# Performance work log

Measured on AMD Instinct MI355X. Metric: run time of the kernel, lower is better.

The kernel has to match this reference:

```python
import jax, jax.numpy as jnp
import numpy as np

B, T, D = 4096, 200, 64
H1, H2 = 128, 64


def setup_inputs() -> dict:
    key = jax.random.key(0)
    ks = jax.random.split(key, 9)
    def glorot(k, shape):
        fan_in, fan_out = shape[0], shape[1]
        lim = float(np.sqrt(6.0 / (fan_in + fan_out)))
        return jax.random.uniform(k, shape, jnp.float32, -lim, lim)
    return {
        "candidate_embedding": jax.random.normal(ks[0], (B, D), jnp.float32),
        "history_embeddings": jax.random.normal(ks[1], (B, T, D), jnp.float32),
        "mask": jax.random.randint(ks[2], (B, T), 0, 2, jnp.int32),
        "W1": glorot(ks[3], (4 * D, H1)),
        "b1": jnp.zeros((H1,), jnp.float32),
        "W2": glorot(ks[4], (H1, H2)),
        "b2": jnp.zeros((H2,), jnp.float32),
        "W3": glorot(ks[5], (H2, 1)),
        "b3": jnp.zeros((1,), jnp.float32),
    }


def reference(candidate_embedding, history_embeddings, mask, W1, b1, W2, b2, W3, b3):
    # candidate: [B, D] -> broadcast to [B, T, D]
    cand = candidate_embedding[:, None, :]  # [B, 1, D]
    cand = jnp.broadcast_to(cand, history_embeddings.shape)
    # DIN feature concat: [B, T, 4D]
    feats = jnp.concatenate(
        [cand, history_embeddings, cand - history_embeddings, cand * history_embeddings],
        axis=-1,
    )
    # small MLP scorer per position
    h = jax.nn.relu(jnp.einsum("btf,fh->bth", feats, W1) + b1)
    h = jax.nn.relu(jnp.einsum("btf,fh->bth", h, W2) + b2)
    scores = (jnp.einsum("btf,fo->bto", h, W3) + b3)[..., 0]  # [B, T]
    # masked softmax over T
    scores = jnp.where(mask == 0, jnp.float32(-1e9), scores)
    weights = jax.nn.softmax(scores, axis=1)  # [B, T]
    # weighted sum over history: [B, D]
    return jnp.einsum("btd,bt->bd", history_embeddings, weights)
```

## Files before the change

kernel.cpp:

```cpp
#include <hip/hip_runtime.h>
#include <hip/hip_bf16.h>

#define NB 4096
#define NT 200
#define ND 64
#define NH1 128
#define NH2 64

#define WS_WX 0
#define WS_WC 16384
#define WS_W2 24576
#define WS_B1 32768
#define WS_B2 32896
#define WS_W3 32960
#define WS_B3 33024

__device__ __align__(16) float  g_wxt[8192];
__device__ __align__(16) float  g_wdt[8192];
__device__ __align__(16) __bf16 g_w2ts[8192];
__device__ __align__(16) __bf16 g_w2tsh[8192];
__device__ __align__(16) __bf16 g_w2tsl[8192];

typedef __bf16 bf16x8 __attribute__((ext_vector_type(8)));
typedef __bf16 bf16x4 __attribute__((ext_vector_type(4)));
typedef float  f32x4  __attribute__((ext_vector_type(4)));

__device__ __forceinline__ float ldany(const void* p, int i, int bf) {
    if (bf) return __bfloat162float(((const __hip_bfloat16*)p)[i]);
    return ((const float*)p)[i];
}

__global__ __launch_bounds__(256) void prep_kernel(
    const void* W1, const void* b1, const void* W2, const void* b2,
    const void* W3, const void* b3, int* flag_out, float* F) {
    __shared__ int votes;
    int tid = threadIdx.x;
    if (tid == 0) votes = 0;
    __syncthreads();
    {
        const unsigned* w1u = (const unsigned*)W1;
        unsigned w = w1u[tid];
        unsigned lo = w & 0xFFFFu;
        unsigned e = (lo >> 7) & 0xFFu;
        if (lo == 0u || (e >= 96u && e <= 124u)) atomicAdd(&votes, 1);
    }
    __syncthreads();
    int bf = (votes >= 160) ? 1 : 0;
    if (blockIdx.x == 0 && tid == 0) flag_out[0] = bf;

    int gtid = blockIdx.x * blockDim.x + tid;
    int gstride = gridDim.x * blockDim.x;

    for (int e = gtid; e < 8192; e += gstride) {
        int k = e >> 7, j = e & 127;
        float w1b = ldany(W1, (64 + k) * 128 + j, bf);
        float w1c = ldany(W1, (128 + k) * 128 + j, bf);
        float w1a = ldany(W1, k * 128 + j, bf);
        float w1d = ldany(W1, (192 + k) * 128 + j, bf);
        float wx = w1b - w1c;
        F[WS_WX + e] = wx;
        F[WS_WX + 8192 + e] = w1d;
        F[WS_WC + e] = w1a + w1c;
        g_wxt[j * 64 + k] = wx;
        g_wdt[j * 64 + k] = w1d;
        float w2v = ldany(W2, e, bf);
        F[WS_W2 + e] = w2v;
        int j2 = e & 63, k2 = e >> 6;
        int so = j2 * 128 + (k2 ^ ((j2 & 15) << 3));
        g_w2ts[so] = (__bf16)w2v;
        __bf16 w2h = (__bf16)w2v;
        g_w2tsh[so] = w2h;
        g_w2tsl[so] = (__bf16)(w2v - (float)w2h);
    }
    for (int e = gtid; e < 128; e += gstride) F[WS_B1 + e] = ldany(b1, e, bf);
    for (int e = gtid; e < 64; e += gstride) {
        F[WS_B2 + e] = ldany(b2, e, bf);
        F[WS_W3 + e] = ldany(W3, e, bf);
    }
    if (gtid == 0) F[WS_B3] = ldany(b3, 0, bf);
}

__device__ __forceinline__ void compute_chunk_bf(
    int w, int lane, int tbase, int b, const int* mask,
    const __bf16* sH, const __bf16* sWhi, const __bf16* sWlo,
    __bf16* h1hi, __bf16* h1lo,
    const float* cbias, const float* b2s, const float* W3s, float b3v,
    float* ss)
{
    const int lq = lane >> 4, lr = lane & 15;
    const int t0 = 16 * w;
    const int ar = t0 + lr;
    const int asw = (ar & 7) << 3;
    const bf16x8 a0 = *(const bf16x8*)&sH[ar * 64 + ((lq * 8) ^ asw)];
    const bf16x8 a1 = *(const bf16x8*)&sH[ar * 64 + ((32 + lq * 8) ^ asw)];
    __syncthreads();

    f32x4 acc2[4];
#pragma unroll
    for (int n = 0; n < 4; n++) {
        const float bb = b2s[n * 16 + lr];
        acc2[n] = (f32x4){bb, bb, bb, bb};
    }

#pragma unroll
    for (int half = 0; half < 2; half++) {
#pragma unroll
        for (int n = 0; n < 4; n++) {
            const int col = half * 64 + n * 16 + lr;
            const int bsw = (col & 7) << 3;
            const int wb = col * 64;
            const float cb = cbias[col];
            f32x4 c = {cb, cb, cb, cb};
            const bf16x8 bh0 = *(const bf16x8*)&sWhi[wb + ((lq * 8) ^ bsw)];
            const bf16x8 bh1 = *(const bf16x8*)&sWhi[wb + ((32 + lq * 8) ^ bsw)];
            const bf16x8 bl0 = *(const bf16x8*)&sWlo[wb + ((lq * 8) ^ bsw)];
            const bf16x8 bl1 = *(const bf16x8*)&sWlo[wb + ((32 + lq * 8) ^ bsw)];
            c = __builtin_amdgcn_mfma_f32_16x16x32_bf16(a0, bh0, c, 0, 0, 0);
            c = __builtin_amdgcn_mfma_f32_16x16x32_bf16(a1, bh1, c, 0, 0, 0);
            c = __builtin_amdgcn_mfma_f32_16x16x32_bf16(a0, bl0, c, 0, 0, 0);
            c = __builtin_amdgcn_mfma_f32_16x16x32_bf16(a1, bl1, c, 0, 0, 0);
#pragma unroll
            for (int r = 0; r < 4; r++) {
                const int row = t0 + lq * 4 + r;
                const int lcol = n * 16 + lr;
                const int hoff = row * 64 + (lcol ^ ((row & 7) << 3));
                float v = fmaxf(c[r], 0.f);
                __bf16 hi = (__bf16)v;
                h1hi[hoff] = hi;
                h1lo[hoff] = (__bf16)(v - (float)hi);
            }
        }
        __syncthreads();
#pragma unroll
        for (int s = 0; s < 2; s++) {
            const int kl = s * 32 + lq * 8;
            const int kg = half * 64 + kl;
            const int hoff2 = (t0 + lr) * 64 + (kl ^ ((lr & 7) << 3));
            const bf16x8 ah = *(const bf16x8*)&h1hi[hoff2];
            const bf16x8 al = *(const bf16x8*)&h1lo[hoff2];
#pragma unroll
            for (int n = 0; n < 4; n++) {
                const int col = n * 16 + lr;
                const int gso = col * 128 + (kg ^ ((col & 15) << 3));
                const bf16x8 bb = *(const bf16x8*)&g_w2ts[gso];
                acc2[n] = __builtin_amdgcn_mfma_f32_16x16x32_bf16(ah, bb, acc2[n], 0, 0, 0);
                acc2[n] = __builtin_amdgcn_mfma_f32_16x16x32_bf16(al, bb, acc2[n], 0, 0, 0);
            }
        }
        if (half == 0) __syncthreads();
    }

#pragma unroll
    for (int r = 0; r < 4; r++) {
        float p = 0.f;
#pragma unroll
        for (int n = 0; n < 4; n++)
            p = fmaf(fmaxf(acc2[n][r], 0.f), W3s[n * 16 + lr], p);
        p += __shfl_xor(p, 1);
        p += __shfl_xor(p, 2);
        p += __shfl_xor(p, 4);
        p += __shfl_xor(p, 8);
        const int gt = tbase + t0 + lq * 4 + r;
        if (lr == 0 && gt < NT)
            ss[gt] = (mask[(long)b * NT + gt] != 0) ? (p + b3v) : -1e9f;
    }
}

__global__ __launch_bounds__(512, 4) void attn_bf16_kernel(
    const void* cand, const void* hist, const int* mask,
    const int* flag_p, const float* F, void* out)
{
    if (flag_p[0] == 0) return;

    __shared__ __align__(16) __bf16 sWhi[8192];
    __shared__ __align__(16) __bf16 sWlo[8192];
    __shared__ __align__(16) __bf16 uBuf[16384];
    __shared__ float cbias[128];
    __shared__ float cs[64], W3s[64], b2s[64];
    __shared__ float ss[NT];
    __shared__ float sred[8];
    __shared__ float b3s;

    const int tid = threadIdx.x;
    const int b = blockIdx.x;
    const int w = tid >> 6, lane = tid & 63;
    const __hip_bfloat16* hp = (const __hip_bfloat16*)hist;

    __bf16* sH = uBuf;
    __bf16* h1hi = uBuf;
    __bf16* h1lo = uBuf + 8192;

    if (tid < 64) {
        cs[tid] = __bfloat162float(((const __hip_bfloat16*)cand)[(long)b * 64 + tid]);
        W3s[tid] = F[WS_W3 + tid];
        b2s[tid] = F[WS_B2 + tid];
    }
    if (tid == 0) b3s = F[WS_B3];
#pragma unroll
    for (int i = 0; i < 2; i++) {
        const int idx = tid + i * 512;
        const int t = idx >> 3, q = idx & 7;
        uint4 v = *(const uint4*)(hp + ((long)b * NT + t) * 64 + q * 8);
        *(uint4*)&sH[t * 64 + ((q * 8) ^ ((t & 7) << 3))] = v;
    }
    __syncthreads();

#pragma unroll
    for (int i = 0; i < 4; i++) {
        const int e4 = tid + i * 512;
        const int j = e4 >> 4, k4 = (e4 & 15) << 2;
        const float4 wx = *(const float4*)&g_wxt[e4 * 4];
        const float4 wd = *(const float4*)&g_wdt[e4 * 4];
        bf16x4 hi4, lo4;
        float v0 = fmaf(cs[k4 + 0], wd.x, wx.x);
        float v1 = fmaf(cs[k4 + 1], wd.y, wx.y);
        float v2 = fmaf(cs[k4 + 2], wd.z, wx.z);
        float v3 = fmaf(cs[k4 + 3], wd.w, wx.w);
        hi4[0] = (__bf16)v0; lo4[0] = (__bf16)(v0 - (float)hi4[0]);
        hi4[1] = (__bf16)v1; lo4[1] = (__bf16)(v1 - (float)hi4[1]);
        hi4[2] = (__bf16)v2; lo4[2] = (__bf16)(v2 - (float)hi4[2]);
        hi4[3] = (__bf16)v3; lo4[3] = (__bf16)(v3 - (float)hi4[3]);
        const int off = j * 64 + (k4 ^ ((j & 7) << 3));
        *(bf16x4*)&sWhi[off] = hi4;
        *(bf16x4*)&sWlo[off] = lo4;
    }
    {
        const int j = tid >> 2, kq = (tid & 3) << 4;
        float a = 0.f;
#pragma unroll
        for (int k2 = 0; k2 < 16; k2++)
            a = fmaf(cs[kq + k2], F[WS_WC + (kq + k2) * 128 + j], a);
        a += __shfl_xor(a, 1);
        a += __shfl_xor(a, 2);
        if ((tid & 3) == 0) cbias[j] = a + F[WS_B1 + j];
    }
    uint4 c1a, c1b = {0, 0, 0, 0};
    {
        const int t = 128 + (tid >> 3), q = tid & 7;
        c1a = *(const uint4*)(hp + ((long)b * NT + t) * 64 + q * 8);
    }
    if (tid < 64) {
        const int t = 192 + (tid >> 3), q = tid & 7;
        c1b = *(const uint4*)(hp + ((long)b * NT + t) * 64 + q * 8);
    }
    __builtin_amdgcn_sched_barrier(0);
    __syncthreads();

    const float b3v = b3s;
    compute_chunk_bf(w, lane, 0, b, mask, sH, sWhi, sWlo, h1hi, h1lo,
                     cbias, b2s, W3s, b3v, ss);
    __syncthreads();

    {
        const int t = tid >> 3, q = tid & 7;
        *(uint4*)&sH[t * 64 + ((q * 8) ^ ((t & 7) << 3))] = c1a;
    }
    if (tid < 64) {
        const int t = 64 + (tid >> 3), q = tid & 7;
        *(uint4*)&sH[t * 64 + ((q * 8) ^ ((t & 7) << 3))] = c1b;
    }
    if (tid < 64) {
        const int t = 72 + (tid >> 3), q = tid & 7;
        uint4 z = {0, 0, 0, 0};
        *(uint4*)&sH[t * 64 + ((q * 8) ^ ((t & 7) << 3))] = z;
    }
    __syncthreads();

    compute_chunk_bf(w, lane, 128, b, mask, sH, sWhi, sWlo, h1hi, h1lo,
                     cbias, b2s, W3s, b3v, ss);
    __syncthreads();

    float v = (tid < NT) ? ss[tid] : -3.0e38f;
    if (tid < 256) {
        float m = v;
#pragma unroll
        for (int o = 32; o; o >>= 1) m = fmaxf(m, __shfl_xor(m, o));
        if ((tid & 63) == 0) sred[tid >> 6] = m;
    }
    __syncthreads();
    const float M = fmaxf(fmaxf(sred[0], sred[1]), fmaxf(sred[2], sred[3]));
    float p = (tid < NT) ? __expf(v - M) : 0.f;
    if (tid < 256) {
        float s2 = p;
#pragma unroll
        for (int o = 32; o; o >>= 1) s2 += __shfl_xor(s2, o);
        if ((tid & 63) == 0) sred[4 + (tid >> 6)] = s2;
    }
    __syncthreads();
    const float S = sred[4] + sred[5] + sred[6] + sred[7];
    if (tid < NT) ss[tid] = p / S;
    __syncthreads();

    float* part = (float*)uBuf;
    const int d = tid & 63, g = tid >> 6;
    float acc = 0.f;
    for (int t = g; t < NT; t += 8)
        acc = fmaf(ss[t], __bfloat162float(hp[((long)b * NT + t) * 64 + d]), acc);
    part[g * 65 + d] = acc;
    __syncthreads();
    if (tid < 64) {
        float o = 0.f;
#pragma unroll
        for (int g2 = 0; g2 < 8; g2++) o += part[g2 * 65 + tid];
        ((__hip_bfloat16*)out)[b * 64 + tid] = __float2bfloat16(o);
    }
}

__device__ __forceinline__ void compute_chunk_f32(
    int w, int lane, int tbase, int b, const int* mask,
    const __bf16* sHhi, const __bf16* sHlo,
    const __bf16* sWhi, const __bf16* sWlo,
    __bf16* h1hi, __bf16* h1lo,
    const float* cbias, const float* b2s, const float* W3s, float b3v,
    float* ss)
{
    const int lq = lane >> 4, lr = lane & 15;
    const int t0 = 16 * w;
    const int ar = t0 + lr;
    const int asw = (ar & 7) << 3;
    const bf16x8 a0h = *(const bf16x8*)&sHhi[ar * 64 + ((lq * 8) ^ asw)];
    const bf16x8 a1h = *(const bf16x8*)&sHhi[ar * 64 + ((32 + lq * 8) ^ asw)];
    const bf16x8 a0l = *(const bf16x8*)&sHlo[ar * 64 + ((lq * 8) ^ asw)];
    const bf16x8 a1l = *(const bf16x8*)&sHlo[ar * 64 + ((32 + lq * 8) ^ asw)];
    __syncthreads();

    f32x4 acc2[4];
#pragma unroll
    for (int n = 0; n < 4; n++) {
        const float bb = b2s[n * 16 + lr];
        acc2[n] = (f32x4){bb, bb, bb, bb};
    }

#pragma unroll
    for (int half = 0; half < 2; half++) {
#pragma unroll
        for (int n = 0; n < 4; n++) {
            const int col = half * 64 + n * 16 + lr;
            const int bsw = (col & 7) << 3;
            const int wb = col * 64;
            const float cb = cbias[col];
            f32x4 c = {cb, cb, cb, cb};
            const bf16x8 bh0 = *(const bf16x8*)&sWhi[wb + ((lq * 8) ^ bsw)];
            const bf16x8 bh1 = *(const bf16x8*)&sWhi[wb + ((32 + lq * 8) ^ bsw)];
            const bf16x8 bl0 = *(const bf16x8*)&sWlo[wb + ((lq * 8) ^ bsw)];
            const bf16x8 bl1 = *(const bf16x8*)&sWlo[wb + ((32 + lq * 8) ^ bsw)];
            c = __builtin_amdgcn_mfma_f32_16x16x32_bf16(a0h, bh0, c, 0, 0, 0);
            c = __builtin_amdgcn_mfma_f32_16x16x32_bf16(a1h, bh1, c, 0, 0, 0);
            c = __builtin_amdgcn_mfma_f32_16x16x32_bf16(a0l, bh0, c, 0, 0, 0);
            c = __builtin_amdgcn_mfma_f32_16x16x32_bf16(a1l, bh1, c, 0, 0, 0);
            c = __builtin_amdgcn_mfma_f32_16x16x32_bf16(a0h, bl0, c, 0, 0, 0);
            c = __builtin_amdgcn_mfma_f32_16x16x32_bf16(a1h, bl1, c, 0, 0, 0);
#pragma unroll
            for (int r = 0; r < 4; r++) {
                const int row = t0 + lq * 4 + r;
                const int lcol = n * 16 + lr;
                const int hoff = row * 64 + (lcol ^ ((row & 7) << 3));
                float v = fmaxf(c[r], 0.f);
                __bf16 hi = (__bf16)v;
                h1hi[hoff] = hi;
                h1lo[hoff] = (__bf16)(v - (float)hi);
            }
        }
        __syncthreads();
#pragma unroll
        for (int s = 0; s < 2; s++) {
            const int kl = s * 32 + lq * 8;
            const int kg = half * 64 + kl;
            const int hoff2 = (t0 + lr) * 64 + (kl ^ ((lr & 7) << 3));
            const bf16x8 ah = *(const bf16x8*)&h1hi[hoff2];
            const bf16x8 al = *(const bf16x8*)&h1lo[hoff2];
#pragma unroll
            for (int n = 0; n < 4; n++) {
                const int col = n * 16 + lr;
                const int gso = col * 128 + (kg ^ ((col & 15) << 3));
                const bf16x8 bh = *(const bf16x8*)&g_w2tsh[gso];
                const bf16x8 bl = *(const bf16x8*)&g_w2tsl[gso];
                acc2[n] = __builtin_amdgcn_mfma_f32_16x16x32_bf16(ah, bh, acc2[n], 0, 0, 0);
                acc2[n] = __builtin_amdgcn_mfma_f32_16x16x32_bf16(al, bh, acc2[n], 0, 0, 0);
                acc2[n] = __builtin_amdgcn_mfma_f32_16x16x32_bf16(ah, bl, acc2[n], 0, 0, 0);
            }
        }
        if (half == 0) __syncthreads();
    }

#pragma unroll
    for (int r = 0; r < 4; r++) {
        float p = 0.f;
#pragma unroll
        for (int n = 0; n < 4; n++)
            p = fmaf(fmaxf(acc2[n][r], 0.f), W3s[n * 16 + lr], p);
        p += __shfl_xor(p, 1);
        p += __shfl_xor(p, 2);
        p += __shfl_xor(p, 4);
        p += __shfl_xor(p, 8);
        const int gt = tbase + t0 + lq * 4 + r;
        if (lr == 0 && gt < NT)
            ss[gt] = (mask[(long)b * NT + gt] != 0) ? (p + b3v) : -1e9f;
    }
}

__global__ __launch_bounds__(512, 4) void attn_f32_kernel(
    const void* cand, const void* hist, const int* mask,
    const int* flag_p, const float* F, void* out)
{
    if (flag_p[0] != 0) return;

    __shared__ __align__(16) __bf16 sWhi[8192];
    __shared__ __align__(16) __bf16 sWlo[8192];
    __shared__ __align__(16) __bf16 uBuf[16384];
    __shared__ float cbias[128];
    __shared__ float cs[64], W3s[64], b2s[64];
    __shared__ float ss[NT];
    __shared__ float sred[8];
    __shared__ float b3s;

    const int tid = threadIdx.x;
    const int b = blockIdx.x;
    const int w = tid >> 6, lane = tid & 63;
    const float* hf = (const float*)hist;

    __bf16* sHhi = uBuf;
    __bf16* sHlo = uBuf + 8192;
    __bf16* h1hi = uBuf;
    __bf16* h1lo = uBuf + 8192;

    if (tid < 64) {
        cs[tid] = ((const float*)cand)[(long)b * 64 + tid];
        W3s[tid] = F[WS_W3 + tid];
        b2s[tid] = F[WS_B2 + tid];
    }
    if (tid == 0) b3s = F[WS_B3];
#pragma unroll
    for (int i = 0; i < 4; i++) {
        const int e4 = tid + i * 512;
        const int t = e4 >> 4, k = (e4 & 15) * 4;
        float4 v = *(const float4*)&hf[((long)b * NT + t) * 64 + k];
        bf16x4 hi4, lo4;
        hi4[0] = (__bf16)v.x; lo4[0] = (__bf16)(v.x - (float)hi4[0]);
        hi4[1] = (__bf16)v.y; lo4[1] = (__bf16)(v.y - (float)hi4[1]);
        hi4[2] = (__bf16)v.z; lo4[2] = (__bf16)(v.z - (float)hi4[2]);
        hi4[3] = (__bf16)v.w; lo4[3] = (__bf16)(v.w - (float)hi4[3]);
        const int pos = ((k & 56) ^ ((t & 7) << 3)) | (k & 4);
        *(bf16x4*)&sHhi[t * 64 + pos] = hi4;
        *(bf16x4*)&sHlo[t * 64 + pos] = lo4;
    }
    __syncthreads();

#pragma unroll
    for (int i = 0; i < 4; i++) {
        const int e4 = tid + i * 512;
        const int j = e4 >> 4, k4 = (e4 & 15) << 2;
        const float4 wx = *(const float4*)&g_wxt[e4 * 4];
        const float4 wd = *(const float4*)&g_wdt[e4 * 4];
        bf16x4 hi4, lo4;
        float v0 = fmaf(cs[k4 + 0], wd.x, wx.x);
        float v1 = fmaf(cs[k4 + 1], wd.y, wx.y);
        float v2 = fmaf(cs[k4 + 2], wd.z, wx.z);
        float v3 = fmaf(cs[k4 + 3], wd.w, wx.w);
        hi4[0] = (__bf16)v0; lo4[0] = (__bf16)(v0 - (float)hi4[0]);
        hi4[1] = (__bf16)v1; lo4[1] = (__bf16)(v1 - (float)hi4[1]);
        hi4[2] = (__bf16)v2; lo4[2] = (__bf16)(v2 - (float)hi4[2]);
        hi4[3] = (__bf16)v3; lo4[3] = (__bf16)(v3 - (float)hi4[3]);
        const int off = j * 64 + (k4 ^ ((j & 7) << 3));
        *(bf16x4*)&sWhi[off] = hi4;
        *(bf16x4*)&sWlo[off] = lo4;
    }
    {
        const int j = tid >> 2, kq = (tid & 3) << 4;
        float a = 0.f;
#pragma unroll
        for (int k2 = 0; k2 < 16; k2++)
            a = fmaf(cs[kq + k2], F[WS_WC + (kq + k2) * 128 + j], a);
        a += __shfl_xor(a, 1);
        a += __shfl_xor(a, 2);
        if ((tid & 3) == 0) cbias[j] = a + F[WS_B1 + j];
    }
    float4 c1a0, c1a1, c1b = {0.f, 0.f, 0.f, 0.f};
    {
        int e4 = tid;
        int tl = e4 >> 4, k = (e4 & 15) * 4;
        c1a0 = *(const float4*)&hf[((long)b * NT + 128 + tl) * 64 + k];
        e4 = tid + 512;
        tl = e4 >> 4; k = (e4 & 15) * 4;
        c1a1 = *(const float4*)&hf[((long)b * NT + 128 + tl) * 64 + k];
    }
    if (tid < 128) {
        const int e4 = 1024 + tid;
        const int tl = e4 >> 4, k = (e4 & 15) * 4;
        c1b = *(const float4*)&hf[((long)b * NT + 128 + tl) * 64 + k];
    }
    __builtin_amdgcn_sched_barrier(0);
    __syncthreads();

    const float b3v = b3s;
    compute_chunk_f32(w, lane, 0, b, mask, sHhi, sHlo, sWhi, sWlo,
                      h1hi, h1lo, cbias, b2s, W3s, b3v, ss);
    __syncthreads();

    {
        int e4 = tid;
        int tl = e4 >> 4, k = (e4 & 15) * 4;
        int pos = ((k & 56) ^ ((tl & 7) << 3)) | (k & 4);
        bf16x4 hi4, lo4;
        hi4[0] = (__bf16)c1a0.x; lo4[0] = (__bf16)(c1a0.x - (float)hi4[0]);
        hi4[1] = (__bf16)c1a0.y; lo4[1] = (__bf16)(c1a0.y - (float)hi4[1]);
        hi4[2] = (__bf16)c1a0.z; lo4[2] = (__bf16)(c1a0.z - (float)hi4[2]);
        hi4[3] = (__bf16)c1a0.w; lo4[3] = (__bf16)(c1a0.w - (float)hi4[3]);
        *(bf16x4*)&sHhi[tl * 64 + pos] = hi4;
        *(bf16x4*)&sHlo[tl * 64 + pos] = lo4;
        e4 = tid + 512;
        tl = e4 >> 4; k = (e4 & 15) * 4;
        pos = ((k & 56) ^ ((tl & 7) << 3)) | (k & 4);
        hi4[0] = (__bf16)c1a1.x; lo4[0] = (__bf16)(c1a1.x - (float)hi4[0]);
        hi4[1] = (__bf16)c1a1.y; lo4[1] = (__bf16)(c1a1.y - (float)hi4[1]);
        hi4[2] = (__bf16)c1a1.z; lo4[2] = (__bf16)(c1a1.z - (float)hi4[2]);
        hi4[3] = (__bf16)c1a1.w; lo4[3] = (__bf16)(c1a1.w - (float)hi4[3]);
        *(bf16x4*)&sHhi[tl * 64 + pos] = hi4;
        *(bf16x4*)&sHlo[tl * 64 + pos] = lo4;
    }
    if (tid < 128) {
        const int e4 = 1024 + tid;
        const int tl = e4 >> 4, k = (e4 & 15) * 4;
        const int pos = ((k & 56) ^ ((tl & 7) << 3)) | (k & 4);
        bf16x4 hi4, lo4;
        hi4[0] = (__bf16)c1b.x; lo4[0] = (__bf16)(c1b.x - (float)hi4[0]);
        hi4[1] = (__bf16)c1b.y; lo4[1] = (__bf16)(c1b.y - (float)hi4[1]);
        hi4[2] = (__bf16)c1b.z; lo4[2] = (__bf16)(c1b.z - (float)hi4[2]);
        hi4[3] = (__bf16)c1b.w; lo4[3] = (__bf16)(c1b.w - (float)hi4[3]);
        *(bf16x4*)&sHhi[tl * 64 + pos] = hi4;
        *(bf16x4*)&sHlo[tl * 64 + pos] = lo4;
    }
    if (tid < 128) {
        const int tl = 72 + (tid >> 4), k = (tid & 15) * 4;
        const int pos = ((k & 56) ^ ((tl & 7) << 3)) | (k & 4);
        bf16x4 z;
        z[0] = (__bf16)0.f; z[1] = (__bf16)0.f; z[2] = (__bf16)0.f; z[3] = (__bf16)0.f;
        *(bf16x4*)&sHhi[tl * 64 + pos] = z;
        *(bf16x4*)&sHlo[tl * 64 + pos] = z;
    }
    __syncthreads();

    compute_chunk_f32(w, lane, 128, b, mask, sHhi, sHlo, sWhi, sWlo,
                      h1hi, h1lo, cbias, b2s, W3s, b3v, ss);
    __syncthreads();

    float v = (tid < NT) ? ss[tid] : -3.0e38f;
    if (tid < 256) {
        float m = v;
#pragma unroll
        for (int o = 32; o; o >>= 1) m = fmaxf(m, __shfl_xor(m, o));
        if ((tid & 63) == 0) sred[tid >> 6] = m;
    }
    __syncthreads();
    const float M = fmaxf(fmaxf(sred[0], sred[1]), fmaxf(sred[2], sred[3]));
    float p = (tid < NT) ? __expf(v - M) : 0.f;
    if (tid < 256) {
        float s2 = p;
#pragma unroll
        for (int o = 32; o; o >>= 1) s2 += __shfl_xor(s2, o);
        if ((tid & 63) == 0) sred[4 + (tid >> 6)] = s2;
    }
    __syncthreads();
    const float S = sred[4] + sred[5] + sred[6] + sred[7];
    if (tid < NT) ss[tid] = p / S;
    __syncthreads();

    float* part = (float*)uBuf;
    const int d = tid & 63, g = tid >> 6;
    float acc = 0.f;
    for (int t = g; t < NT; t += 8)
        acc = fmaf(ss[t], hf[((long)b * NT + t) * 64 + d], acc);
    part[g * 65 + d] = acc;
    __syncthreads();
    if (tid < 64) {
        float o = 0.f;
#pragma unroll
        for (int g2 = 0; g2 < 8; g2++) o += part[g2 * 65 + tid];
        ((float*)out)[b * 64 + tid] = o;
    }
}

extern "C" void kernel_launch(void* const* d_in, const int* in_sizes, int n_in,
                              void* d_out, int out_size, void* d_ws, size_t ws_size,
                              hipStream_t stream) {
    const void* cand = d_in[0];
    const void* hist = d_in[1];
    const int* mask = (const int*)d_in[2];
    const void* W1 = d_in[3];
    const void* b1 = d_in[4];
    const void* W2 = d_in[5];
    const void* b2 = d_in[6];
    const void* W3 = d_in[7];
    const void* b3 = d_in[8];

    int* flag = (int*)d_ws;
    float* F = (float*)((char*)d_ws + 256);

    prep_kernel<<<32, 256, 0, stream>>>(W1, b1, W2, b2, W3, b3, flag, F);
    attn_f32_kernel<<<NB, 512, 0, stream>>>(cand, hist, mask, flag, F, d_out);
    attn_bf16_kernel<<<NB, 512, 0, stream>>>(cand, hist, mask, flag, F, d_out);
}
```

Baseline: 611.0 us.

## Shrink blocks to 256 threads and process history in 64-row chunks with prefetch

Both attention kernels drop from 512 to 256 threads per block and walk the 200 history rows in four 64-row chunks instead of two 128-row chunks. The next chunk is prefetched from global memory into registers while the current chunk's MLP runs. Shared memory for the activation buffer is halved and launch bounds change to (256,3), aiming at more resident blocks per CU and better latency hiding. The cost is more barriers per block and serial chunk iterations within each block.

New measurement: 776.1 us. 1.27x slower.

```diff
diff --git a/kernel.cpp b/kernel.cpp
--- a/kernel.cpp
+++ b/kernel.cpp
@@ -80,93 +80,7 @@
     if (gtid == 0) F[WS_B3] = ldany(b3, 0, bf);
 }
 
-__device__ __forceinline__ void compute_chunk_bf(
-    int w, int lane, int tbase, int b, const int* mask,
-    const __bf16* sH, const __bf16* sWhi, const __bf16* sWlo,
-    __bf16* h1hi, __bf16* h1lo,
-    const float* cbias, const float* b2s, const float* W3s, float b3v,
-    float* ss)
-{
-    const int lq = lane >> 4, lr = lane & 15;
-    const int t0 = 16 * w;
-    const int ar = t0 + lr;
-    const int asw = (ar & 7) << 3;
-    const bf16x8 a0 = *(const bf16x8*)&sH[ar * 64 + ((lq * 8) ^ asw)];
-    const bf16x8 a1 = *(const bf16x8*)&sH[ar * 64 + ((32 + lq * 8) ^ asw)];
-    __syncthreads();
-
-    f32x4 acc2[4];
-#pragma unroll
-    for (int n = 0; n < 4; n++) {
-        const float bb = b2s[n * 16 + lr];
-        acc2[n] = (f32x4){bb, bb, bb, bb};
-    }
-
-#pragma unroll
-    for (int half = 0; half < 2; half++) {
-#pragma unroll
-        for (int n = 0; n < 4; n++) {
-            const int col = half * 64 + n * 16 + lr;
-            const int bsw = (col & 7) << 3;
-            const int wb = col * 64;
-            const float cb = cbias[col];
-            f32x4 c = {cb, cb, cb, cb};
-            const bf16x8 bh0 = *(const bf16x8*)&sWhi[wb + ((lq * 8) ^ bsw)];
-            const bf16x8 bh1 = *(const bf16x8*)&sWhi[wb + ((32 + lq * 8) ^ bsw)];
-            const bf16x8 bl0 = *(const bf16x8*)&sWlo[wb + ((lq * 8) ^ bsw)];
-            const bf16x8 bl1 = *(const bf16x8*)&sWlo[wb + ((32 + lq * 8) ^ bsw)];
-            c = __builtin_amdgcn_mfma_f32_16x16x32_bf16(a0, bh0, c, 0, 0, 0);
-            c = __builtin_amdgcn_mfma_f32_16x16x32_bf16(a1, bh1, c, 0, 0, 0);
-            c = __builtin_amdgcn_mfma_f32_16x16x32_bf16(a0, bl0, c, 0, 0, 0);
-            c = __builtin_amdgcn_mfma_f32_16x16x32_bf16(a1, bl1, c, 0, 0, 0);
-#pragma unroll
-            for (int r = 0; r < 4; r++) {
-                const int row = t0 + lq * 4 + r;
-                const int lcol = n * 16 + lr;
-                const int hoff = row * 64 + (lcol ^ ((row & 7) << 3));
-                float v = fmaxf(c[r], 0.f);
-                __bf16 hi = (__bf16)v;
-                h1hi[hoff] = hi;
-                h1lo[hoff] = (__bf16)(v - (float)hi);
-            }
-        }
-        __syncthreads();
-#pragma unroll
-        for (int s = 0; s < 2; s++) {
-            const int kl = s * 32 + lq * 8;
-            const int kg = half * 64 + kl;
-            const int hoff2 = (t0 + lr) * 64 + (kl ^ ((lr & 7) << 3));
-            const bf16x8 ah = *(const bf16x8*)&h1hi[hoff2];
-            const bf16x8 al = *(const bf16x8*)&h1lo[hoff2];
-#pragma unroll
-            for (int n = 0; n < 4; n++) {
-                const int col = n * 16 + lr;
-                const int gso = col * 128 + (kg ^ ((col & 15) << 3));
-                const bf16x8 bb = *(const bf16x8*)&g_w2ts[gso];
-                acc2[n] = __builtin_amdgcn_mfma_f32_16x16x32_bf16(ah, bb, acc2[n], 0, 0, 0);
-                acc2[n] = __builtin_amdgcn_mfma_f32_16x16x32_bf16(al, bb, acc2[n], 0, 0, 0);
-            }
-        }
-        if (half == 0) __syncthreads();
-    }
-
-#pragma unroll
-    for (int r = 0; r < 4; r++) {
-        float p = 0.f;
-#pragma unroll
-        for (int n = 0; n < 4; n++)
-            p = fmaf(fmaxf(acc2[n][r], 0.f), W3s[n * 16 + lr], p);
-        p += __shfl_xor(p, 1);
-        p += __shfl_xor(p, 2);
-        p += __shfl_xor(p, 4);
-        p += __shfl_xor(p, 8);
-        const int gt = tbase + t0 + lq * 4 + r;
-        if (lr == 0 && gt < NT)
-            ss[gt] = (mask[(long)b * NT + gt] != 0) ? (p + b3v) : -1e9f;
-    }
-}
-
-__global__ __launch_bounds__(512, 4) void attn_bf16_kernel(
+__global__ __launch_bounds__(256, 3) void attn_bf16_kernel(
     const void* cand, const void* hist, const int* mask,
     const int* flag_p, const float* F, void* out)
 {
@@ -174,7 +88,7 @@
 
     __shared__ __align__(16) __bf16 sWhi[8192];
     __shared__ __align__(16) __bf16 sWlo[8192];
-    __shared__ __align__(16) __bf16 uBuf[16384];
+    __shared__ __align__(16) __bf16 uBuf[8192];
     __shared__ float cbias[128];
     __shared__ float cs[64], W3s[64], b2s[64];
     __shared__ float ss[NT];
@@ -184,11 +98,12 @@
     const int tid = threadIdx.x;
     const int b = blockIdx.x;
     const int w = tid >> 6, lane = tid & 63;
+    const int lq = lane >> 4, lr = lane & 15;
     const __hip_bfloat16* hp = (const __hip_bfloat16*)hist;
 
     __bf16* sH = uBuf;
     __bf16* h1hi = uBuf;
-    __bf16* h1lo = uBuf + 8192;
+    __bf16* h1lo = uBuf + 4096;
 
     if (tid < 64) {
         cs[tid] = __bfloat162float(((const __hip_bfloat16*)cand)[(long)b * 64 + tid]);
@@ -198,7 +113,7 @@
     if (tid == 0) b3s = F[WS_B3];
 #pragma unroll
     for (int i = 0; i < 2; i++) {
-        const int idx = tid + i * 512;
+        const int idx = tid + i * 256;
         const int t = idx >> 3, q = idx & 7;
         uint4 v = *(const uint4*)(hp + ((long)b * NT + t) * 64 + q * 8);
         *(uint4*)&sH[t * 64 + ((q * 8) ^ ((t & 7) << 3))] = v;
@@ -206,8 +121,8 @@
     __syncthreads();
 
 #pragma unroll
-    for (int i = 0; i < 4; i++) {
-        const int e4 = tid + i * 512;
+    for (int i = 0; i < 8; i++) {
+        const int e4 = tid + i * 256;
         const int j = e4 >> 4, k4 = (e4 & 15) << 2;
         const float4 wx = *(const float4*)&g_wxt[e4 * 4];
         const float4 wd = *(const float4*)&g_wdt[e4 * 4];
@@ -225,66 +140,145 @@
         *(bf16x4*)&sWlo[off] = lo4;
     }
     {
-        const int j = tid >> 2, kq = (tid & 3) << 4;
+        const int j = tid >> 1, kq = (tid & 1) << 5;
         float a = 0.f;
 #pragma unroll
-        for (int k2 = 0; k2 < 16; k2++)
+        for (int k2 = 0; k2 < 32; k2++)
             a = fmaf(cs[kq + k2], F[WS_WC + (kq + k2) * 128 + j], a);
         a += __shfl_xor(a, 1);
-        a += __shfl_xor(a, 2);
-        if ((tid & 3) == 0) cbias[j] = a + F[WS_B1 + j];
-    }
-    uint4 c1a, c1b = {0, 0, 0, 0};
-    {
-        const int t = 128 + (tid >> 3), q = tid & 7;
-        c1a = *(const uint4*)(hp + ((long)b * NT + t) * 64 + q * 8);
-    }
-    if (tid < 64) {
-        const int t = 192 + (tid >> 3), q = tid & 7;
-        c1b = *(const uint4*)(hp + ((long)b * NT + t) * 64 + q * 8);
-    }
-    __builtin_amdgcn_sched_barrier(0);
+        if ((tid & 1) == 0) cbias[j] = a + F[WS_B1 + j];
+    }
     __syncthreads();
 
     const float b3v = b3s;
-    compute_chunk_bf(w, lane, 0, b, mask, sH, sWhi, sWlo, h1hi, h1lo,
-                     cbias, b2s, W3s, b3v, ss);
-    __syncthreads();
-
-    {
-        const int t = tid >> 3, q = tid & 7;
-        *(uint4*)&sH[t * 64 + ((q * 8) ^ ((t & 7) << 3))] = c1a;
-    }
-    if (tid < 64) {
-        const int t = 64 + (tid >> 3), q = tid & 7;
-        *(uint4*)&sH[t * 64 + ((q * 8) ^ ((t & 7) << 3))] = c1b;
-    }
-    if (tid < 64) {
-        const int t = 72 + (tid >> 3), q = tid & 7;
-        uint4 z = {0, 0, 0, 0};
-        *(uint4*)&sH[t * 64 + ((q * 8) ^ ((t & 7) << 3))] = z;
-    }
-    __syncthreads();
-
-    compute_chunk_bf(w, lane, 128, b, mask, sH, sWhi, sWlo, h1hi, h1lo,
-                     cbias, b2s, W3s, b3v, ss);
-    __syncthreads();
+    uint4 pf0 = {0, 0, 0, 0}, pf1 = {0, 0, 0, 0};
+
+    for (int c = 0; c < 4; ++c) {
+        const int tbase = c * 64;
+        const int ar = 16 * w + lr;
+        const int asw = (ar & 7) << 3;
+        const bf16x8 a0 = *(const bf16x8*)&sH[ar * 64 + ((lq * 8) ^ asw)];
+        const bf16x8 a1 = *(const bf16x8*)&sH[ar * 64 + ((32 + lq * 8) ^ asw)];
+        __syncthreads();
+
+        if (c < 3) {
+            {
+                const int t = tid >> 3, q = tid & 7;
+                const int row = tbase + 64 + t;
+                uint4 zz = {0, 0, 0, 0};
+                pf0 = (row < NT)
+                    ? *(const uint4*)(hp + ((long)b * NT + row) * 64 + q * 8) : zz;
+            }
+            {
+                const int idx = tid + 256;
+                const int t = idx >> 3, q = idx & 7;
+                const int row = tbase + 64 + t;
+                uint4 zz = {0, 0, 0, 0};
+                pf1 = (row < NT)
+                    ? *(const uint4*)(hp + ((long)b * NT + row) * 64 + q * 8) : zz;
+            }
+        }
+
+        f32x4 acc2[4];
+#pragma unroll
+        for (int n = 0; n < 4; n++) {
+            const float bb = b2s[n * 16 + lr];
+            acc2[n] = (f32x4){bb, bb, bb, bb};
+        }
+
+#pragma unroll
+        for (int half = 0; half < 2; half++) {
+#pragma unroll
+            for (int n = 0; n < 4; n++) {
+                const int col = half * 64 + n * 16 + lr;
+                const int bsw = (col & 7) << 3;
+                const int wb = col * 64;
+                const float cb = cbias[col];
+                f32x4 cc = {cb, cb, cb, cb};
+                const bf16x8 bh0 = *(const bf16x8*)&sWhi[wb + ((lq * 8) ^ bsw)];
+                const bf16x8 bh1 = *(const bf16x8*)&sWhi[wb + ((32 + lq * 8) ^ bsw)];
+                const bf16x8 bl0 = *(const bf16x8*)&sWlo[wb + ((lq * 8) ^ bsw)];
+                const bf16x8 bl1 = *(const bf16x8*)&sWlo[wb + ((32 + lq * 8) ^ bsw)];
+                cc = __builtin_amdgcn_mfma_f32_16x16x32_bf16(a0, bh0, cc, 0, 0, 0);
+                cc = __builtin_amdgcn_mfma_f32_16x16x32_bf16(a1, bh1, cc, 0, 0, 0);
+                cc = __builtin_amdgcn_mfma_f32_16x16x32_bf16(a0, bl0, cc, 0, 0, 0);
+                cc = __builtin_amdgcn_mfma_f32_16x16x32_bf16(a1, bl1, cc, 0, 0, 0);
+#pragma unroll
+                for (int r = 0; r < 4; r++) {
+                    const int row = 16 * w + lq * 4 + r;
+                    const int lcol = n * 16 + lr;
+                    const int hoff = row * 64 + (lcol ^ ((row & 7) << 3));
+                    float v = fmaxf(cc[r], 0.f);
+                    __bf16 hi = (__bf16)v;
+                    h1hi[hoff] = hi;
+                    h1lo[hoff] = (__bf16)(v - (float)hi);
+                }
+            }
+            __syncthreads();
+#pragma unroll
+            for (int s = 0; s < 2; s++) {
+                const int kl = s * 32 + lq * 8;
+                const int kg = half * 64 + kl;
+                const int hoff2 = (16 * w + lr) * 64 + (kl ^ ((lr & 7) << 3));
+                const bf16x8 ah = *(const bf16x8*)&h1hi[hoff2];
+                const bf16x8 al = *(const bf16x8*)&h1lo[hoff2];
+#pragma unroll
+                for (int n = 0; n < 4; n++) {
+                    const int col = n * 16 + lr;
+                    const int gso = col * 128 + (kg ^ ((col & 15) << 3));
+                    const bf16x8 bb = *(const bf16x8*)&g_w2ts[gso];
+                    acc2[n] = __builtin_amdgcn_mfma_f32_16x16x32_bf16(ah, bb, acc2[n], 0, 0, 0);
+                    acc2[n] = __builtin_amdgcn_mfma_f32_16x16x32_bf16(al, bb, acc2[n], 0, 0, 0);
+                }
+            }
+            if (half == 0) __syncthreads();
+        }
+
+#pragma unroll
+        for (int r = 0; r < 4; r++) {
+            float p = 0.f;
+#pragma unroll
+            for (int n = 0; n < 4; n++)
+                p = fmaf(fmaxf(acc2[n][r], 0.f), W3s[n * 16 + lr], p);
+            p += __shfl_xor(p, 1);
+            p += __shfl_xor(p, 2);
+            p += __shfl_xor(p, 4);
+            p += __shfl_xor(p, 8);
+            const int gt = tbase + 16 * w + lq * 4 + r;
+            if (lr == 0 && gt < NT)
+                ss[gt] = (mask[(long)b * NT + gt] != 0) ? (p + b3v) : -1e9f;
+        }
+        __syncthreads();
+
+        if (c < 3) {
+            {
+                const int t = tid >> 3, q = tid & 7;
+                *(uint4*)&sH[t * 64 + ((q * 8) ^ ((t & 7) << 3))] = pf0;
+            }
+            {
+                const int idx = tid + 256;
+                const int t = idx >> 3, q = idx & 7;
+                *(uint4*)&sH[t * 64 + ((q * 8) ^ ((t & 7) << 3))] = pf1;
+            }
+            __syncthreads();
+        }
+    }
 
     float v = (tid < NT) ? ss[tid] : -3.0e38f;
-    if (tid < 256) {
+    {
         float m = v;
 #pragma unroll
         for (int o = 32; o; o >>= 1) m = fmaxf(m, __shfl_xor(m, o));
-        if ((tid & 63) == 0) sred[tid >> 6] = m;
+        if (lane == 0) sred[w] = m;
     }
     __syncthreads();
     const float M = fmaxf(fmaxf(sred[0], sred[1]), fmaxf(sred[2], sred[3]));
     float p = (tid < NT) ? __expf(v - M) : 0.f;
-    if (tid < 256) {
+    {
         float s2 = p;
 #pragma unroll
         for (int o = 32; o; o >>= 1) s2 += __shfl_xor(s2, o);
-        if ((tid & 63) == 0) sred[4 + (tid >> 6)] = s2;
+        if (lane == 0) sred[4 + w] = s2;
     }
     __syncthreads();
     const float S = sred[4] + sred[5] + sred[6] + sred[7];
@@ -292,114 +286,21 @@
     __syncthreads();
 
     float* part = (float*)uBuf;
-    const int d = tid & 63, g = tid >> 6;
+    const int d = tid & 63;
     float acc = 0.f;
-    for (int t = g; t < NT; t += 8)
+    for (int t = w; t < NT; t += 4)
         acc = fmaf(ss[t], __bfloat162float(hp[((long)b * NT + t) * 64 + d]), acc);
-    part[g * 65 + d] = acc;
+    part[w * 65 + d] = acc;
     __syncthreads();
     if (tid < 64) {
         float o = 0.f;
 #pragma unroll
-        for (int g2 = 0; g2 < 8; g2++) o += part[g2 * 65 + tid];
+        for (int g2 = 0; g2 < 4; g2++) o += part[g2 * 65 + tid];
         ((__hip_bfloat16*)out)[b * 64 + tid] = __float2bfloat16(o);
     }
 }
 
-__device__ __forceinline__ void compute_chunk_f32(
-    int w, int lane, int tbase, int b, const int* mask,
-    const __bf16* sHhi, const __bf16* sHlo,
-    const __bf16* sWhi, const __bf16* sWlo,
-    __bf16* h1hi, __bf16* h1lo,
-    const float* cbias, const float* b2s, const float* W3s, float b3v,
-    float* ss)
-{
-    const int lq = lane >> 4, lr = lane & 15;
-    const int t0 = 16 * w;
-    const int ar = t0 + lr;
-    const int asw = (ar & 7) << 3;
-    const bf16x8 a0h = *(const bf16x8*)&sHhi[ar * 64 + ((lq * 8) ^ asw)];
-    const bf16x8 a1h = *(const bf16x8*)&sHhi[ar * 64 + ((32 + lq * 8) ^ asw)];
-    const bf16x8 a0l = *(const bf16x8*)&sHlo[ar * 64 + ((lq * 8) ^ asw)];
-    const bf16x8 a1l = *(const bf16x8*)&sHlo[ar * 64 + ((32 + lq * 8) ^ asw)];
-    __syncthreads();
-
-    f32x4 acc2[4];
-#pragma unroll
-    for (int n = 0; n < 4; n++) {
-        const float bb = b2s[n * 16 + lr];
-        acc2[n] = (f32x4){bb, bb, bb, bb};
-    }
-
-#pragma unroll
-    for (int half = 0; half < 2; half++) {
-#pragma unroll
-        for (int n = 0; n < 4; n++) {
-            const int col = half * 64 + n * 16 + lr;
-            const int bsw = (col & 7) << 3;
-            const int wb = col * 64;
-            const float cb = cbias[col];
-            f32x4 c = {cb, cb, cb, cb};
-            const bf16x8 bh0 = *(const bf16x8*)&sWhi[wb + ((lq * 8) ^ bsw)];
-            const bf16x8 bh1 = *(const bf16x8*)&sWhi[wb + ((32 + lq * 8) ^ bsw)];
-            const bf16x8 bl0 = *(const bf16x8*)&sWlo[wb + ((lq * 8) ^ bsw)];
-            const bf16x8 bl1 = *(const bf16x8*)&sWlo[wb + ((32 + lq * 8) ^ bsw)];
-            c = __builtin_amdgcn_mfma_f32_16x16x32_bf16(a0h, bh0, c, 0, 0, 0);
-            c = __builtin_amdgcn_mfma_f32_16x16x32_bf16(a1h, bh1, c, 0, 0, 0);
-            c = __builtin_amdgcn_mfma_f32_16x16x32_bf16(a0l, bh0, c, 0, 0, 0);
-            c = __builtin_amdgcn_mfma_f32_16x16x32_bf16(a1l, bh1, c, 0, 0, 0);
-            c = __builtin_amdgcn_mfma_f32_16x16x32_bf16(a0h, bl0, c, 0, 0, 0);
-            c = __builtin_amdgcn_mfma_f32_16x16x32_bf16(a1h, bl1, c, 0, 0, 0);
-#pragma unroll
-            for (int r = 0; r < 4; r++) {
-                const int row = t0 + lq * 4 + r;
-                const int lcol = n * 16 + lr;
-                const int hoff = row * 64 + (lcol ^ ((row & 7) << 3));
-                float v = fmaxf(c[r], 0.f);
-                __bf16 hi = (__bf16)v;
-                h1hi[hoff] = hi;
-                h1lo[hoff] = (__bf16)(v - (float)hi);
-            }
-        }
-        __syncthreads();
-#pragma unroll
-        for (int s = 0; s < 2; s++) {
-            const int kl = s * 32 + lq * 8;
-            const int kg = half * 64 + kl;
-            const int hoff2 = (t0 + lr) * 64 + (kl ^ ((lr & 7) << 3));
-            const bf16x8 ah = *(const bf16x8*)&h1hi[hoff2];
-            const bf16x8 al = *(const bf16x8*)&h1lo[hoff2];
-#pragma unroll
-            for (int n = 0; n < 4; n++) {
-                const int col = n * 16 + lr;
-                const int gso = col * 128 + (kg ^ ((col & 15) << 3));
-                const bf16x8 bh = *(const bf16x8*)&g_w2tsh[gso];
-                const bf16x8 bl = *(const bf16x8*)&g_w2tsl[gso];
-                acc2[n] = __builtin_amdgcn_mfma_f32_16x16x32_bf16(ah, bh, acc2[n], 0, 0, 0);
-                acc2[n] = __builtin_amdgcn_mfma_f32_16x16x32_bf16(al, bh, acc2[n], 0, 0, 0);
-                acc2[n] = __builtin_amdgcn_mfma_f32_16x16x32_bf16(ah, bl, acc2[n], 0, 0, 0);
-            }
-        }
-        if (half == 0) __syncthreads();
-    }
-
-#pragma unroll
-    for (int r = 0; r < 4; r++) {
-        float p = 0.f;
-#pragma unroll
-        for (int n = 0; n < 4; n++)
-            p = fmaf(fmaxf(acc2[n][r], 0.f), W3s[n * 16 + lr], p);
-        p += __shfl_xor(p, 1);
-        p += __shfl_xor(p, 2);
-        p += __shfl_xor(p, 4);
-        p += __shfl_xor(p, 8);
-        const int gt = tbase + t0 + lq * 4 + r;
-        if (lr == 0 && gt < NT)
-            ss[gt] = (mask[(long)b * NT + gt] != 0) ? (p + b3v) : -1e9f;
-    }
-}
-
-__global__ __launch_bounds__(512, 4) void attn_f32_kernel(
+__global__ __launch_bounds__(256, 3) void attn_f32_kernel(
     const void* cand, const void* hist, const int* mask,
     const int* flag_p, const float* F, void* out)
 {
@@ -407,7 +308,7 @@
 
     __shared__ __align__(16) __bf16 sWhi[8192];
     __shared__ __align__(16) __bf16 sWlo[8192];
-    __shared__ __align__(16) __bf16 uBuf[16384];
+    __shared__ __align__(16) __bf16 uBuf[8192];
     __shared__ float cbias[128];
     __shared__ float cs[64], W3s[64], b2s[64];
     __shared__ float ss[NT];
@@ -417,12 +318,13 @@
     const int tid = threadIdx.x;
     const int b = blockIdx.x;
     const int w = tid >> 6, lane = tid & 63;
+    const int lq = lane >> 4, lr = lane & 15;
     const float* hf = (const float*)hist;
 
     __bf16* sHhi = uBuf;
-    __bf16* sHlo = uBuf + 8192;
+    __bf16* sHlo = uBuf + 4096;
     __bf16* h1hi = uBuf;
-    __bf16* h1lo = uBuf + 8192;
+    __bf16* h1lo = uBuf + 4096;
 
     if (tid < 64) {
         cs[tid] = ((const float*)cand)[(long)b * 64 + tid];
@@ -432,7 +334,7 @@
     if (tid == 0) b3s = F[WS_B3];
 #pragma unroll
     for (int i = 0; i < 4; i++) {
-        const int e4 = tid + i * 512;
+        const int e4 = tid + i * 256;
         const int t = e4 >> 4, k = (e4 & 15) * 4;
         float4 v = *(const float4*)&hf[((long)b * NT + t) * 64 + k];
         bf16x4 hi4, lo4;
@@ -447,8 +349,8 @@
     __syncthreads();
 
 #pragma unroll
-    for (int i = 0; i < 4; i++) {
-        const int e4 = tid + i * 512;
+    for (int i = 0; i < 8; i++) {
+        const int e4 = tid + i * 256;
         const int j = e4 >> 4, k4 = (e4 & 15) << 2;
         const float4 wx = *(const float4*)&g_wxt[e4 * 4];
         const float4 wd = *(const float4*)&g_wdt[e4 * 4];
@@ -466,99 +368,152 @@
         *(bf16x4*)&sWlo[off] = lo4;
     }
     {
-        const int j = tid >> 2, kq = (tid & 3) << 4;
+        const int j = tid >> 1, kq = (tid & 1) << 5;
         float a = 0.f;
 #pragma unroll
-        for (int k2 = 0; k2 < 16; k2++)
+        for (int k2 = 0; k2 < 32; k2++)
             a = fmaf(cs[kq + k2], F[WS_WC + (kq + k2) * 128 + j], a);
         a += __shfl_xor(a, 1);
-        a += __shfl_xor(a, 2);
-        if ((tid & 3) == 0) cbias[j] = a + F[WS_B1 + j];
-    }
-    float4 c1a0, c1a1, c1b = {0.f, 0.f, 0.f, 0.f};
-    {
-        int e4 = tid;
-        int tl = e4 >> 4, k = (e4 & 15) * 4;
-        c1a0 = *(const float4*)&hf[((long)b * NT + 128 + tl) * 64 + k];
-        e4 = tid + 512;
-        tl = e4 >> 4; k = (e4 & 15) * 4;
-        c1a1 = *(const float4*)&hf[((long)b * NT + 128 + tl) * 64 + k];
-    }
-    if (tid < 128) {
-        const int e4 = 1024 + tid;
-        const int tl = e4 >> 4, k = (e4 & 15) * 4;
-        c1b = *(const float4*)&hf[((long)b * NT + 128 + tl) * 64 + k];
-    }
-    __builtin_amdgcn_sched_barrier(0);
+        if ((tid & 1) == 0) cbias[j] = a + F[WS_B1 + j];
+    }
     __syncthreads();
 
     const float b3v = b3s;
-    compute_chunk_f32(w, lane, 0, b, mask, sHhi, sHlo, sWhi, sWlo,
-                      h1hi, h1lo, cbias, b2s, W3s, b3v, ss);
-    __syncthreads();
-
-    {
-        int e4 = tid;
-        int tl = e4 >> 4, k = (e4 & 15) * 4;
-        int pos = ((k & 56) ^ ((tl & 7) << 3)) | (k & 4);
-        bf16x4 hi4, lo4;
-        hi4[0] = (__bf16)c1a0.x; lo4[0] = (__bf16)(c1a0.x - (float)hi4[0]);
-        hi4[1] = (__bf16)c1a0.y; lo4[1] = (__bf16)(c1a0.y - (float)hi4[1]);
-        hi4[2] = (__bf16)c1a0.z; lo4[2] = (__bf16)(c1a0.z - (float)hi4[2]);
-        hi4[3] = (__bf16)c1a0.w; lo4[3] = (__bf16)(c1a0.w - (float)hi4[3]);
-        *(bf16x4*)&sHhi[tl * 64 + pos] = hi4;
-        *(bf16x4*)&sHlo[tl * 64 + pos] = lo4;
-        e4 = tid + 512;
-        tl = e4 >> 4; k = (e4 & 15) * 4;
-        pos = ((k & 56) ^ ((tl & 7) << 3)) | (k & 4);
-        hi4[0] = (__bf16)c1a1.x; lo4[0] = (__bf16)(c1a1.x - (float)hi4[0]);
-        hi4[1] = (__bf16)c1a1.y; lo4[1] = (__bf16)(c1a1.y - (float)hi4[1]);
-        hi4[2] = (__bf16)c1a1.z; lo4[2] = (__bf16)(c1a1.z - (float)hi4[2]);
-        hi4[3] = (__bf16)c1a1.w; lo4[3] = (__bf16)(c1a1.w - (float)hi4[3]);
-        *(bf16x4*)&sHhi[tl * 64 + pos] = hi4;
-        *(bf16x4*)&sHlo[tl * 64 + pos] = lo4;
-    }
-    if (tid < 128) {
-        const int e4 = 1024 + tid;
-        const int tl = e4 >> 4, k = (e4 & 15) * 4;
-        const int pos = ((k & 56) ^ ((tl & 7) << 3)) | (k & 4);
-        bf16x4 hi4, lo4;
-        hi4[0] = (__bf16)c1b.x; lo4[0] = (__bf16)(c1b.x - (float)hi4[0]);
-        hi4[1] = (__bf16)c1b.y; lo4[1] = (__bf16)(c1b.y - (float)hi4[1]);
-        hi4[2] = (__bf16)c1b.z; lo4[2] = (__bf16)(c1b.z - (float)hi4[2]);
-        hi4[3] = (__bf16)c1b.w; lo4[3] = (__bf16)(c1b.w - (float)hi4[3]);
-        *(bf16x4*)&sHhi[tl * 64 + pos] = hi4;
-        *(bf16x4*)&sHlo[tl * 64 + pos] = lo4;
-    }
-    if (tid < 128) {
-        const int tl = 72 + (tid >> 4), k = (tid & 15) * 4;
-        const int pos = ((k & 56) ^ ((tl & 7) << 3)) | (k & 4);
-        bf16x4 z;
-        z[0] = (__bf16)0.f; z[1] = (__bf16)0.f; z[2] = (__bf16)0.f; z[3] = (__bf16)0.f;
-        *(bf16x4*)&sHhi[tl * 64 + pos] = z;
-        *(bf16x4*)&sHlo[tl * 64 + pos] = z;
-    }
-    __syncthreads();
-
-    compute_chunk_f32(w, lane, 128, b, mask, sHhi, sHlo, sWhi, sWlo,
-                      h1hi, h1lo, cbias, b2s, W3s, b3v, ss);
-    __syncthreads();
+    float4 pf[4];
+#pragma unroll
+    for (int i = 0; i < 4; i++) pf[i] = (float4){0.f, 0.f, 0.f, 0.f};
+
+    for (int c = 0; c < 4; ++c) {
+        const int tbase = c * 64;
+        const int ar = 16 * w + lr;
+        const int asw = (ar & 7) << 3;
+        const bf16x8 a0h = *(const bf16x8*)&sHhi[ar * 64 + ((lq * 8) ^ asw)];
+        const bf16x8 a1h = *(const bf16x8*)&sHhi[ar * 64 + ((32 + lq * 8) ^ asw)];
+        const bf16x8 a0l = *(const bf16x8*)&sHlo[ar * 64 + ((lq * 8) ^ asw)];
+        const bf16x8 a1l = *(const bf16x8*)&sHlo[ar * 64 + ((32 + lq * 8) ^ asw)];
+        __syncthreads();
+
+        if (c < 3) {
+#pragma unroll
+            for (int i = 0; i < 4; i++) {
+                const int e4 = tid + i * 256;
+                const int t = e4 >> 4, k = (e4 & 15) * 4;
+                const int row = tbase + 64 + t;
+                float4 zz = {0.f, 0.f, 0.f, 0.f};
+                pf[i] = (row < NT)
+                    ? *(const float4*)&hf[((long)b * NT + row) * 64 + k] : zz;
+            }
+        }
+
+        f32x4 acc2[4];
+#pragma unroll
+        for (int n = 0; n < 4; n++) {
+            const float bb = b2s[n * 16 + lr];
+            acc2[n] = (f32x4){bb, bb, bb, bb};
+        }
+
+#pragma unroll
+        for (int half = 0; half < 2; half++) {
+#pragma unroll
+            for (int n = 0; n < 4; n++) {
+                const int col = half * 64 + n * 16 + lr;
+                const int bsw = (col & 7) << 3;
+                const int wb = col * 64;
+                const float cb = cbias[col];
+                f32x4 cc = {cb, cb, cb, cb};
+                const bf16x8 bh0 = *(const bf16x8*)&sWhi[wb + ((lq * 8) ^ bsw)];
+                const bf16x8 bh1 = *(const bf16x8*)&sWhi[wb + ((32 + lq * 8) ^ bsw)];
+                const bf16x8 bl0 = *(const bf16x8*)&sWlo[wb + ((lq * 8) ^ bsw)];
+                const bf16x8 bl1 = *(const bf16x8*)&sWlo[wb + ((32 + lq * 8) ^ bsw)];
+                cc = __builtin_amdgcn_mfma_f32_16x16x32_bf16(a0h, bh0, cc, 0, 0, 0);
+                cc = __builtin_amdgcn_mfma_f32_16x16x32_bf16(a1h, bh1, cc, 0, 0, 0);
+                cc = __builtin_amdgcn_mfma_f32_16x16x32_bf16(a0l, bh0, cc, 0, 0, 0);
+                cc = __builtin_amdgcn_mfma_f32_16x16x32_bf16(a1l, bh1, cc, 0, 0, 0);
+                cc = __builtin_amdgcn_mfma_f32_16x16x32_bf16(a0h, bl0, cc, 0, 0, 0);
+                cc = __builtin_amdgcn_mfma_f32_16x16x32_bf16(a1h, bl1, cc, 0, 0, 0);
+#pragma unroll
+                for (int r = 0; r < 4; r++) {
+                    const int row = 16 * w + lq * 4 + r;
+                    const int lcol = n * 16 + lr;
+                    const int hoff = row * 64 + (lcol ^ ((row & 7) << 3));
+                    float v = fmaxf(cc[r], 0.f);
+                    __bf16 hi = (__bf16)v;
+                    h1hi[hoff] = hi;
+                    h1lo[hoff] = (__bf16)(v - (float)hi);
+                }
+            }
+            __syncthreads();
+#pragma unroll
+            for (int s = 0; s < 2; s++) {
+                const int kl = s * 32 + lq * 8;
+                const int kg = half * 64 + kl;
+                const int hoff2 = (16 * w + lr) * 64 + (kl ^ ((lr & 7) << 3));
+                const bf16x8 ah = *(const bf16x8*)&h1hi[hoff2];
+                const bf16x8 al = *(const bf16x8*)&h1lo[hoff2];
+#pragma unroll
+                for (int n = 0; n < 4; n++) {
+                    const int col = n * 16 + lr;
+                    const int gso = col * 128 + (kg ^ ((col & 15) << 3));
+                    const bf16x8 bh = *(const bf16x8*)&g_w2tsh[gso];
+                    const bf16x8 bl = *(const bf16x8*)&g_w2tsl[gso];
+                    acc2[n] = __builtin_amdgcn_mfma_f32_16x16x32_bf16(ah, bh, acc2[n], 0, 0, 0);
+                    acc2[n] = __builtin_amdgcn_mfma_f32_16x16x32_bf16(al, bh, acc2[n], 0, 0, 0);
+                    acc2[n] = __builtin_amdgcn_mfma_f32_16x16x32_bf16(ah, bl, acc2[n], 0, 0, 0);
+                }
+            }
+            if (half == 0) __syncthreads();
+        }
+
+#pragma unroll
+        for (int r = 0; r < 4; r++) {
+            float p = 0.f;
+#pragma unroll
+            for (int n = 0; n < 4; n++)
+                p = fmaf(fmaxf(acc2[n][r], 0.f), W3s[n * 16 + lr], p);
+            p += __shfl_xor(p, 1);
+            p += __shfl_xor(p, 2);
+            p += __shfl_xor(p, 4);
+            p += __shfl_xor(p, 8);
+            const int gt = tbase + 16 * w + lq * 4 + r;
+            if (lr == 0 && gt < NT)
+                ss[gt] = (mask[(long)b * NT + gt] != 0) ? (p + b3v) : -1e9f;
+        }
+        __syncthreads();
+
+        if (c < 3) {
+#pragma unroll
+            for (int i = 0; i < 4; i++) {
+                const int e4 = tid + i * 256;
+                const int t = e4 >> 4, k = (e4 & 15) * 4;
+                const float4 vv = pf[i];
+                bf16x4 hi4, lo4;
+                hi4[0] = (__bf16)vv.x; lo4[0] = (__bf16)(vv.x - (float)hi4[0]);
+                hi4[1] = (__bf16)vv.y; lo4[1] = (__bf16)(vv.y - (float)hi4[1]);
+                hi4[2] = (__bf16)vv.z; lo4[2] = (__bf16)(vv.z - (float)hi4[2]);
+                hi4[3] = (__bf16)vv.w; lo4[3] = (__bf16)(vv.w - (float)hi4[3]);
+                const int pos = ((k & 56) ^ ((t & 7) << 3)) | (k & 4);
+                *(bf16x4*)&sHhi[t * 64 + pos] = hi4;
+                *(bf16x4*)&sHlo[t * 64 + pos] = lo4;
+            }
+            __syncthreads();
+        }
+    }
 
     float v = (tid < NT) ? ss[tid] : -3.0e38f;
-    if (tid < 256) {
+    {
         float m = v;
 #pragma unroll
         for (int o = 32; o; o >>= 1) m = fmaxf(m, __shfl_xor(m, o));
-        if ((tid & 63) == 0) sred[tid >> 6] = m;
+        if (lane == 0) sred[w] = m;
     }
     __syncthreads();
     const float M = fmaxf(fmaxf(sred[0], sred[1]), fmaxf(sred[2], sred[3]));
     float p = (tid < NT) ? __expf(v - M) : 0.f;
-    if (tid < 256) {
+    {
         float s2 = p;
 #pragma unroll
         for (int o = 32; o; o >>= 1) s2 += __shfl_xor(s2, o);
-        if ((tid & 63) == 0) sred[4 + (tid >> 6)] = s2;
+        if (lane == 0) sred[4 + w] = s2;
     }
     __syncthreads();
     const float S = sred[4] + sred[5] + sred[6] + sred[7];
@@ -566,16 +521,16 @@
     __syncthreads();
 
     float* part = (float*)uBuf;
-    const int d = tid & 63, g = tid >> 6;
+    const int d = tid & 63;
     float acc = 0.f;
-    for (int t = g; t < NT; t += 8)
+    for (int t = w; t < NT; t += 4)
         acc = fmaf(ss[t], hf[((long)b * NT + t) * 64 + d], acc);
-    part[g * 65 + d] = acc;
+    part[w * 65 + d] = acc;
     __syncthreads();
     if (tid < 64) {
         float o = 0.f;
 #pragma unroll
-        for (int g2 = 0; g2 < 8; g2++) o += part[g2 * 65 + tid];
+        for (int g2 = 0; g2 < 4; g2++) o += part[g2 * 65 + tid];
         ((float*)out)[b * 64 + tid] = o;
     }
 }
@@ -597,6 +552,6 @@
     float* F = (float*)((char*)d_ws + 256);
 
     prep_kernel<<<32, 256, 0, stream>>>(W1, b1, W2, b2, W3, b3, flag, F);
-    attn_f32_kernel<<<NB, 512, 0, stream>>>(cand, hist, mask, flag, F, d_out);
-    attn_bf16_kernel<<<NB, 512, 0, stream>>>(cand, hist, mask, flag, F, d_out);
+    attn_f32_kernel<<<NB, 256, 0, stream>>>(cand, hist, mask, flag, F, d_out);
+    attn_bf16_kernel<<<NB, 256, 0, stream>>>(cand, hist, mask, flag, F, d_out);
 }
```
